# Performance work log

Measured on AMD Instinct MI355X. Metric: run time of the kernel, lower is better.

Reference implementation:

```python
import jax, jax.numpy as jnp
import numpy as np

N_VARS = 200000
M_CONS = 100000
NNZ = 1600000
HID = 128
NEG_SLOPE = 0.01  # torch F.leaky_relu default


def setup_inputs() -> dict:
    key = jax.random.key(0)
    ks = jax.random.split(key, 14)
    s = 0.05
    return {
        "primal": jax.random.normal(ks[0], (N_VARS, HID), jnp.float32),
        "last_primal": jax.random.normal(ks[1], (N_VARS, HID), jnp.float32),
        "dual": jax.random.normal(ks[2], (M_CONS, HID), jnp.float32),
        "rows": jax.random.randint(ks[3], (NNZ,), 0, M_CONS),
        "cols": jax.random.randint(ks[4], (NNZ,), 0, N_VARS),
        "vals": jax.random.normal(ks[5], (NNZ,), jnp.float32),
        "right_hand_side": jax.random.normal(ks[6], (M_CONS, HID), jnp.float32),
        "W1": jax.random.normal(ks[7], (HID, HID), jnp.float32) * s,
        "b1": jax.random.normal(ks[8], (HID,), jnp.float32) * s,
        "W2": jax.random.normal(ks[9], (HID, HID), jnp.float32) * s,
        "b2": jax.random.normal(ks[10], (HID,), jnp.float32) * s,
        "W3": jax.random.normal(ks[11], (HID, HID), jnp.float32) * s,
        "b3": jax.random.normal(ks[12], (HID,), jnp.float32) * s,
        "sigma": jnp.asarray(2.0, jnp.float32),
    }


def reference(primal, last_primal, dual, rows, cols, vals, right_hand_side,
              W1, b1, W2, b2, W3, b3, sigma):
    # X = Theta2(primal) - Theta3(last_primal): [n_vars, hid]
    X = (primal @ W2.T + b2) - (last_primal @ W3.T + b3)
    # sparse.mm(A_coo, X): gather source rows, scale by nnz vals, scatter-add to constraint rows
    msgs = vals[:, None] * X[cols]                      # [nnz, hid]
    AX = jax.ops.segment_sum(msgs, rows, num_segments=M_CONS)  # [m_cons, hid]
    pre = (dual @ W1.T + b1) + sigma * (AX - right_hand_side)
    return jnp.where(pre >= 0, pre, NEG_SLOPE * pre)
```

## Files before the change

kernel.cpp:

```cpp
#include <hip/hip_runtime.h>

#define HID 128
#define NEG_SLOPE 0.01f
#define NB 256
#define CHUNK 2048
#define MAX_RB 512
#define CAP 8192

typedef __attribute__((ext_vector_type(8))) short short8;
typedef __attribute__((ext_vector_type(4))) float f32x4;
typedef __attribute__((ext_vector_type(4))) unsigned u32x4;

__device__ inline unsigned short f2bfu(float f) {
    unsigned u = __float_as_uint(f);
    u += 0x7fff + ((u >> 16) & 1);
    return (unsigned short)(u >> 16);
}
__device__ inline float bf2f_lo(unsigned x) { return __uint_as_float((x & 0xffffu) << 16); }
__device__ inline float bf2f_hi(unsigned x) { return __uint_as_float(x & 0xffff0000u); }

__device__ inline unsigned cvtpk(float lo, float hi) {
    unsigned r;
    asm("v_cvt_pk_bf16_f32 %0, %1, %2" : "=v"(r) : "v"(lo), "v"(hi));
    return r;
}

#define MFMA_SW(accv, wfrag, xfrag) \
    asm("v_mfma_f32_16x16x32_bf16 %0, %1, %2, %0" : "+v"(accv) : "v"(wfrag), "v"(xfrag))

__global__ __launch_bounds__(256) void k_prep(
    const float* __restrict__ W1, const float* __restrict__ W2, const float* __restrict__ W3,
    unsigned short* __restrict__ Wcat, short8* __restrict__ W1F)
{
    int gid = blockIdx.x * 256 + threadIdx.x;
    if (gid < 128 * 256) {
        int n = gid >> 8, k = gid & 255;
        float v = (k < 128) ? W2[n * 128 + k] : -W3[n * 128 + (k - 128)];
        Wcat[gid] = f2bfu(v);
    } else if (gid < 128 * 256 + 2048) {
        int e = gid - 128 * 256;
        int lane = e & 63, ks = (e >> 6) & 3, nb = e >> 8;
        int row = nb * 16 + (lane & 15);
        int k0 = ks * 32 + ((lane >> 4) << 3);
        short8 v;
        #pragma unroll
        for (int j = 0; j < 8; ++j)
            v[j] = (short)f2bfu(W1[row * 128 + k0 + j]);
        W1F[e] = v;
    }
}

__device__ inline void load_a(const float* __restrict__ Ap, long rowbase, int nrows_tot,
                              int rrow, int rcol, float4 (&araw)[2][8])
{
    const float4 z4 = {0.f, 0.f, 0.f, 0.f};
    #pragma unroll
    for (int rg = 0; rg < 2; ++rg) {
        long row = rowbase + rrow + rg * 16;
        const float4* rp = (const float4*)(Ap + row * HID + rcol);
        if (row < nrows_tot) {
            #pragma unroll
            for (int ks = 0; ks < 4; ++ks) {
                araw[rg][ks * 2 + 0] = rp[ks * 8 + 0];
                araw[rg][ks * 2 + 1] = rp[ks * 8 + 1];
            }
        } else {
            #pragma unroll
            for (int u = 0; u < 8; ++u) araw[rg][u] = z4;
        }
    }
}

__device__ inline void conv_a(const float4 (&araw)[2][8], u32x4 (&af)[2][4])
{
    #pragma unroll
    for (int rg = 0; rg < 2; ++rg)
        #pragma unroll
        for (int ks = 0; ks < 4; ++ks) {
            float4 x0 = araw[rg][ks * 2 + 0], x1 = araw[rg][ks * 2 + 1];
            af[rg][ks][0] = cvtpk(x0.x, x0.y);
            af[rg][ks][1] = cvtpk(x0.z, x0.w);
            af[rg][ks][2] = cvtpk(x1.x, x1.y);
            af[rg][ks][3] = cvtpk(x1.z, x1.w);
        }
}

__device__ inline void mfma_half(f32x4 (&acc)[2][8], const u32x4 (&af)[2][4],
                                 const short8* Blds, int base, int l)
{
    #pragma unroll
    for (int ks = 0; ks < 4; ++ks)
        #pragma unroll
        for (int nb = 0; nb < 8; ++nb) {
            short8 bv = Blds[base + (nb * 4 + ks) * 64 + l];
            MFMA_SW(acc[0][nb], bv, af[0][ks]);
            MFMA_SW(acc[1][nb], bv, af[1][ks]);
        }
}

__global__ __launch_bounds__(256, 2) void k_theta_bfill(
    const float* __restrict__ primal, const float* __restrict__ lastp,
    const short8* __restrict__ Wcat,
    const float* __restrict__ b2, const float* __restrict__ b3,
    unsigned short* __restrict__ Xb, int nvars, int ntiles, int tgrid,
    const int* __restrict__ rows, const int* __restrict__ cols, const float* __restrict__ vals,
    int* __restrict__ cursor, int2* __restrict__ tmp_rc, float* __restrict__ tmp_v, int nnz, int rb,
    const float* __restrict__ dual, const short8* __restrict__ W1F,
    const float* __restrict__ b1, const float* __restrict__ rhs,
    const float* __restrict__ sigp, unsigned short* __restrict__ predualb, int mcons, int nchunks)
{
    __shared__ short8 Blds[4096];
    const int t = threadIdx.x;

    if (blockIdx.x < (unsigned)tgrid) {
        const int l = t & 63, wv = t >> 6;
        const int rrow = wv * 32 + (l & 15);
        const int rcol = (l >> 4) << 3;
        const int colb = (l >> 4) << 2;

        float4 araw[2][8];
        const long tile0 = blockIdx.x;
        load_a(primal, tile0 * 128, nvars, rrow, rcol, araw);

        #pragma unroll
        for (int i = 0; i < 16; ++i) {
            int e = t + i * 256;
            int lane = e & 63, ks = (e >> 6) & 3, nb = (e >> 8) & 7, hf = e >> 11;
            int row = nb * 16 + (lane & 15);
            int col8 = (hf * 128 + ks * 32 + ((lane >> 4) << 3)) >> 3;
            Blds[e] = Wcat[row * 32 + col8];
        }

        float4 bias[8];
        #pragma unroll
        for (int nb = 0; nb < 8; ++nb) {
            int col = nb * 16 + colb;
            float4 p = *(const float4*)&b2[col];
            float4 q = *(const float4*)&b3[col];
            bias[nb] = make_float4(p.x - q.x, p.y - q.y, p.z - q.z, p.w - q.w);
        }

        __syncthreads();

        const f32x4 z = {0.f, 0.f, 0.f, 0.f};
        f32x4 acc[2][8];
        #pragma unroll
        for (int rg = 0; rg < 2; ++rg)
            #pragma unroll
            for (int nb = 0; nb < 8; ++nb) acc[rg][nb] = z;

        u32x4 af[2][4];

        #pragma unroll 1
        for (long tile = tile0; tile < ntiles; tile += tgrid) {
            conv_a(araw, af);
            load_a(lastp, tile * 128, nvars, rrow, rcol, araw);
            mfma_half(acc, af, Blds, 0, l);

            conv_a(araw, af);
            long nt = tile + tgrid;
            if (nt < ntiles) load_a(primal, nt * 128, nvars, rrow, rcol, araw);
            mfma_half(acc, af, Blds, 2048, l);

            asm volatile("s_nop 7\ns_nop 7");
            #pragma unroll
            for (int rg = 0; rg < 2; ++rg) {
                long row = tile * 128 + rrow + rg * 16;
                if (row < nvars) {
                    #pragma unroll
                    for (int nb = 0; nb < 8; ++nb) {
                        uint2 w;
                        w.x = cvtpk(acc[rg][nb][0] + bias[nb].x, acc[rg][nb][1] + bias[nb].y);
                        w.y = cvtpk(acc[rg][nb][2] + bias[nb].z, acc[rg][nb][3] + bias[nb].w);
                        *(uint2*)&Xb[row * HID + nb * 16 + colb] = w;
                    }
                }
                #pragma unroll
                for (int nb = 0; nb < 8; ++nb) acc[rg][nb] = z;
            }
        }
    } else if (blockIdx.x < (unsigned)(tgrid + nchunks)) {
        int* hist  = (int*)Blds;
        int* basep = hist + NB;
        int cb = blockIdx.x - tgrid;
        long cbase = (long)cb * CHUNK;
        hist[t] = 0;
        __syncthreads();

        int r[8], c[8], b[8], loc[8];
        float v[8];
        #pragma unroll
        for (int i = 0; i < 8; ++i) {
            long e = cbase + i * 256 + t;
            int locv = -1; int bi = 0; int ri = 0, ci = 0; float vi = 0.f;
            if (e < nnz) {
                ri = rows[e]; ci = cols[e]; vi = vals[e];
                bi = ri / rb;
                locv = atomicAdd(&hist[bi], 1);
            }
            r[i] = ri; c[i] = ci; v[i] = vi; b[i] = bi; loc[i] = locv;
        }
        __syncthreads();
        if (hist[t] > 0) basep[t] = atomicAdd(&cursor[t], hist[t]);
        __syncthreads();
        #pragma unroll
        for (int i = 0; i < 8; ++i) {
            if (loc[i] >= 0) {
                int o = basep[b[i]] + loc[i];
                if (o < CAP) {
                    long slot = (long)b[i] * CAP + o;
                    tmp_rc[slot] = make_int2(r[i], c[i]);
                    tmp_v[slot]  = v[i];
                }
            }
        }
    } else {
        const int l = t & 63, wv = t >> 6;
        const int rrow = wv * 32 + (l & 15);
        const int rcol = (l >> 4) << 3;
        const int colb = (l >> 4) << 2;
        const float sigma = *sigp;
        const long rowbase = (long)(blockIdx.x - tgrid - nchunks) * 128;

        float4 araw[2][8];
        load_a(dual, rowbase, mcons, rrow, rcol, araw);

        u32x4 af[2][4];
        conv_a(araw, af);

        const f32x4 z = {0.f, 0.f, 0.f, 0.f};
        f32x4 acc[2][8];
        #pragma unroll
        for (int rg = 0; rg < 2; ++rg)
            #pragma unroll
            for (int nb = 0; nb < 8; ++nb) acc[rg][nb] = z;

        #pragma unroll
        for (int ks = 0; ks < 4; ++ks)
            #pragma unroll
            for (int nb = 0; nb < 8; ++nb) {
                short8 bv = W1F[(nb * 4 + ks) * 64 + l];
                MFMA_SW(acc[0][nb], bv, af[0][ks]);
                MFMA_SW(acc[1][nb], bv, af[1][ks]);
            }
        asm volatile("s_nop 7\ns_nop 7");

        float4 bias[8];
        #pragma unroll
        for (int nb = 0; nb < 8; ++nb)
            bias[nb] = *(const float4*)&b1[nb * 16 + colb];

        #pragma unroll
        for (int rg = 0; rg < 2; ++rg) {
            long row = rowbase + rrow + rg * 16;
            if (row < mcons) {
                #pragma unroll
                for (int nb = 0; nb < 8; ++nb) {
                    long idx = row * HID + nb * 16 + colb;
                    float4 r4 = *(const float4*)&rhs[idx];
                    uint2 w;
                    w.x = cvtpk(acc[rg][nb][0] + bias[nb].x - sigma * r4.x,
                                acc[rg][nb][1] + bias[nb].y - sigma * r4.y);
                    w.y = cvtpk(acc[rg][nb][2] + bias[nb].z - sigma * r4.z,
                                acc[rg][nb][3] + bias[nb].w - sigma * r4.w);
                    *(uint2*)&predualb[idx] = w;
                }
            }
        }
    }
}

__global__ __launch_bounds__(256) void k_csr(
    const int2* __restrict__ tmp_rc, const float* __restrict__ tmp_v,
    const int* __restrict__ bucket_fill,
    int* __restrict__ rowstart, int* __restrict__ count, int2* __restrict__ pairs,
    int m, int rb)
{
    __shared__ int cnt[MAX_RB];
    __shared__ int cur[MAX_RB];
    int b = blockIdx.x, t = threadIdx.x;
    int row0 = b * rb;
    int nrows = m - row0; if (nrows > rb) nrows = rb;
    if (nrows <= 0) return;

    for (int i = t; i < nrows; i += 256) cnt[i] = 0;
    __syncthreads();

    long e0 = (long)b * CAP;
    int fill = bucket_fill[b]; if (fill > CAP) fill = CAP;
    long e1 = e0 + fill;
    for (long e = e0 + t; e < e1; e += 256)
        atomicAdd(&cnt[tmp_rc[e].x - row0], 1);
    __syncthreads();

    if (t == 0) {
        int run = (int)e0;
        for (int i = 0; i < nrows; ++i) { cur[i] = run; run += cnt[i]; }
    }
    __syncthreads();

    for (int i = t; i < nrows; i += 256) {
        rowstart[row0 + i] = cur[i];
        count[row0 + i]    = cnt[i];
    }
    __syncthreads();

    for (long e = e0 + t; e < e1; e += 256) {
        int2 rc = tmp_rc[e];
        float vv = tmp_v[e];
        int slot = atomicAdd(&cur[rc.x - row0], 1);
        pairs[slot] = make_int2(rc.y, __float_as_int(vv));
    }
}

__global__ __launch_bounds__(256) void k_segsum(
    const int2* __restrict__ pairs, const int* __restrict__ rowstart, const int* __restrict__ count,
    const unsigned short* __restrict__ Xb, const unsigned short* __restrict__ predualb,
    const float* __restrict__ sigp, float* __restrict__ out, int m)
{
    int w = (blockIdx.x * 256 + threadIdx.x) >> 6;
    int lane = threadIdx.x & 63;
    int q = lane >> 4;
    int sub = lane & 15;
    int row = w * 4 + q;
    bool valid = row < m;
    int start = valid ? rowstart[row] : 0;
    int cnt   = valid ? count[row]    : 0;

    int c0 = __shfl(cnt, 0);
    int c1 = __shfl(cnt, 16);
    int c2 = __shfl(cnt, 32);
    int c3 = __shfl(cnt, 48);
    int cmax = max(max(c0, c1), max(c2, c3));

    const unsigned short* xb = Xb + sub * 8;

    float a0 = 0.f, a1 = 0.f, a2 = 0.f, a3 = 0.f;
    float a4 = 0.f, a5 = 0.f, a6 = 0.f, a7 = 0.f;
    for (int j = 0; j < cmax; j += 8) {
        int2 p[8]; u32x4 x[8];
        #pragma unroll
        for (int u = 0; u < 8; ++u) {
            bool act = (j + u) < cnt;
            int2 pv = make_int2(0, 0);
            if (act) pv = pairs[start + j + u];
            p[u] = pv;
        }
        #pragma unroll
        for (int u = 0; u < 8; ++u)
            x[u] = *(const u32x4*)(xb + (size_t)p[u].x * HID);
        #pragma unroll
        for (int u = 0; u < 8; ++u) {
            float v = __int_as_float(p[u].y);
            a0 += v * bf2f_lo(x[u][0]); a1 += v * bf2f_hi(x[u][0]);
            a2 += v * bf2f_lo(x[u][1]); a3 += v * bf2f_hi(x[u][1]);
            a4 += v * bf2f_lo(x[u][2]); a5 += v * bf2f_hi(x[u][2]);
            a6 += v * bf2f_lo(x[u][3]); a7 += v * bf2f_hi(x[u][3]);
        }
    }
    if (valid) {
        float sg = *sigp;
        long base = (size_t)row * HID + sub * 8;
        u32x4 pd = *(const u32x4*)&predualb[base];
        float4 o0, o1;
        o0.x = bf2f_lo(pd[0]) + sg * a0;
        o0.y = bf2f_hi(pd[0]) + sg * a1;
        o0.z = bf2f_lo(pd[1]) + sg * a2;
        o0.w = bf2f_hi(pd[1]) + sg * a3;
        o1.x = bf2f_lo(pd[2]) + sg * a4;
        o1.y = bf2f_hi(pd[2]) + sg * a5;
        o1.z = bf2f_lo(pd[3]) + sg * a6;
        o1.w = bf2f_hi(pd[3]) + sg * a7;
        o0.x = (o0.x >= 0.f) ? o0.x : NEG_SLOPE * o0.x;
        o0.y = (o0.y >= 0.f) ? o0.y : NEG_SLOPE * o0.y;
        o0.z = (o0.z >= 0.f) ? o0.z : NEG_SLOPE * o0.z;
        o0.w = (o0.w >= 0.f) ? o0.w : NEG_SLOPE * o0.w;
        o1.x = (o1.x >= 0.f) ? o1.x : NEG_SLOPE * o1.x;
        o1.y = (o1.y >= 0.f) ? o1.y : NEG_SLOPE * o1.y;
        o1.z = (o1.z >= 0.f) ? o1.z : NEG_SLOPE * o1.z;
        o1.w = (o1.w >= 0.f) ? o1.w : NEG_SLOPE * o1.w;
        *(float4*)&out[base]     = o0;
        *(float4*)&out[base + 4] = o1;
    }
}

extern "C" void kernel_launch(void* const* d_in, const int* in_sizes, int n_in,
                              void* d_out, int out_size, void* d_ws, size_t ws_size,
                              hipStream_t stream) {
    const float* primal = (const float*)d_in[0];
    const float* lastp  = (const float*)d_in[1];
    const float* dual   = (const float*)d_in[2];
    const int*   rows   = (const int*)d_in[3];
    const int*   cols   = (const int*)d_in[4];
    const float* vals   = (const float*)d_in[5];
    const float* rhs    = (const float*)d_in[6];
    const float* W1     = (const float*)d_in[7];
    const float* b1     = (const float*)d_in[8];
    const float* W2     = (const float*)d_in[9];
    const float* b2     = (const float*)d_in[10];
    const float* W3     = (const float*)d_in[11];
    const float* b3     = (const float*)d_in[12];
    const float* sigp   = (const float*)d_in[13];

    const int nvars = in_sizes[0] / HID;
    const int mcons = in_sizes[2] / HID;
    const int nnz   = in_sizes[3];
    const int rb    = (mcons + NB - 1) / NB;

    float* out = (float*)d_out;

    char* wsb = (char*)d_ws;
    unsigned short* Xb = (unsigned short*)wsb;
    size_t off = (size_t)nvars * HID * sizeof(unsigned short);
    int2* pairs   = (int2*)(wsb + off);  off += (size_t)NB * CAP * sizeof(int2);
    int2* tmp_rc  = (int2*)(wsb + off);  off += (size_t)NB * CAP * sizeof(int2);
    float* tmp_v  = (float*)(wsb + off); off += (size_t)NB * CAP * sizeof(float);
    unsigned short* predualb = (unsigned short*)(wsb + off);
    off += (size_t)mcons * HID * sizeof(unsigned short);
    unsigned short* Wcat = (unsigned short*)(wsb + off); off += 128 * 256 * 2;
    short8* W1F   = (short8*)(wsb + off); off += 2048 * sizeof(short8);
    int* count    = (int*)(wsb + off); off += (size_t)mcons * sizeof(int);
    int* rowstart = (int*)(wsb + off); off += (size_t)mcons * sizeof(int);
    int* cursor   = (int*)(wsb + off); off += NB * sizeof(int);

    hipMemsetAsync(cursor, 0, NB * sizeof(int), stream);

    k_prep<<<136, 256, 0, stream>>>(W1, W2, W3, Wcat, W1F);

    const int ntiles = (nvars + 127) / 128;
    const int tgrid = 512;
    const int nchunks = (nnz + CHUNK - 1) / CHUNK;
    const int pblocks = (mcons + 127) / 128;
    k_theta_bfill<<<tgrid + nchunks + pblocks, 256, 0, stream>>>(
        primal, lastp, (const short8*)Wcat, b2, b3, Xb, nvars, ntiles, tgrid,
        rows, cols, vals, cursor, tmp_rc, tmp_v, nnz, rb,
        dual, W1F, b1, rhs, sigp, predualb, mcons, nchunks);

    k_csr<<<NB, 256, 0, stream>>>(tmp_rc, tmp_v, cursor,
                                  rowstart, count, pairs, mcons, rb);

    int nwaves = (mcons + 3) / 4;
    k_segsum<<<(nwaves + 3) / 4, 256, 0, stream>>>(
        pairs, rowstart, count, Xb, predualb, sigp, out, mcons);
}
```

Measured before the change: 218.8 us.

## Fuse CSR build and segment sum into one LDS-bucketed finalize kernel

Measured after the change: 203.6 us. 6.9% less time.

```diff
diff --git a/kernel.cpp b/kernel.cpp
--- a/kernel.cpp
+++ b/kernel.cpp
@@ -2,10 +2,10 @@
 
 #define HID 128
 #define NEG_SLOPE 0.01f
-#define NB 256
+#define NBK 2048
 #define CHUNK 2048
-#define MAX_RB 512
-#define CAP 8192
+#define CAPK 1024
+#define MAX_RB 64
 
 typedef __attribute__((ext_vector_type(8))) short short8;
 typedef __attribute__((ext_vector_type(4))) float f32x4;
@@ -181,10 +181,11 @@
         }
     } else if (blockIdx.x < (unsigned)(tgrid + nchunks)) {
         int* hist  = (int*)Blds;
-        int* basep = hist + NB;
+        int* basep = hist + NBK;
         int cb = blockIdx.x - tgrid;
         long cbase = (long)cb * CHUNK;
-        hist[t] = 0;
+        #pragma unroll
+        for (int i = 0; i < NBK / 256; ++i) hist[t + i * 256] = 0;
         __syncthreads();
 
         int r[8], c[8], b[8], loc[8];
@@ -201,14 +202,18 @@
             r[i] = ri; c[i] = ci; v[i] = vi; b[i] = bi; loc[i] = locv;
         }
         __syncthreads();
-        if (hist[t] > 0) basep[t] = atomicAdd(&cursor[t], hist[t]);
+        #pragma unroll
+        for (int i = 0; i < NBK / 256; ++i) {
+            int bi = t + i * 256;
+            if (hist[bi] > 0) basep[bi] = atomicAdd(&cursor[bi], hist[bi]);
+        }
         __syncthreads();
         #pragma unroll
         for (int i = 0; i < 8; ++i) {
             if (loc[i] >= 0) {
                 int o = basep[b[i]] + loc[i];
-                if (o < CAP) {
-                    long slot = (long)b[i] * CAP + o;
+                if (o < CAPK) {
+                    long slot = (long)b[i] * CAPK + o;
                     tmp_rc[slot] = make_int2(r[i], c[i]);
                     tmp_v[slot]  = v[i];
                 }
@@ -270,117 +275,95 @@
     }
 }
 
-__global__ __launch_bounds__(256) void k_csr(
+__global__ __launch_bounds__(256) void k_segfin(
     const int2* __restrict__ tmp_rc, const float* __restrict__ tmp_v,
-    const int* __restrict__ bucket_fill,
-    int* __restrict__ rowstart, int* __restrict__ count, int2* __restrict__ pairs,
-    int m, int rb)
-{
-    __shared__ int cnt[MAX_RB];
-    __shared__ int cur[MAX_RB];
-    int b = blockIdx.x, t = threadIdx.x;
-    int row0 = b * rb;
+    const int* __restrict__ cursor,
+    const unsigned short* __restrict__ Xb, const unsigned short* __restrict__ predualb,
+    const float* __restrict__ sigp, float* __restrict__ out, int m, int rb)
+{
+    __shared__ int2 pairsL[CAPK];
+    __shared__ int cntL[MAX_RB], startL[MAX_RB], curL[MAX_RB];
+    const int b = blockIdx.x, t = threadIdx.x;
+    const int row0 = b * rb;
     int nrows = m - row0; if (nrows > rb) nrows = rb;
     if (nrows <= 0) return;
-
-    for (int i = t; i < nrows; i += 256) cnt[i] = 0;
+    int fill = cursor[b]; if (fill > CAPK) fill = CAPK;
+    const long e0 = (long)b * CAPK;
+
+    for (int i = t; i < nrows; i += 256) cntL[i] = 0;
     __syncthreads();
-
-    long e0 = (long)b * CAP;
-    int fill = bucket_fill[b]; if (fill > CAP) fill = CAP;
-    long e1 = e0 + fill;
-    for (long e = e0 + t; e < e1; e += 256)
-        atomicAdd(&cnt[tmp_rc[e].x - row0], 1);
+    for (int e = t; e < fill; e += 256)
+        atomicAdd(&cntL[tmp_rc[e0 + e].x - row0], 1);
     __syncthreads();
-
     if (t == 0) {
-        int run = (int)e0;
-        for (int i = 0; i < nrows; ++i) { cur[i] = run; run += cnt[i]; }
+        int run = 0;
+        for (int i = 0; i < nrows; ++i) { startL[i] = run; curL[i] = run; run += cntL[i]; }
     }
     __syncthreads();
-
-    for (int i = t; i < nrows; i += 256) {
-        rowstart[row0 + i] = cur[i];
-        count[row0 + i]    = cnt[i];
+    for (int e = t; e < fill; e += 256) {
+        int2 rc = tmp_rc[e0 + e];
+        float vv = tmp_v[e0 + e];
+        int slot = atomicAdd(&curL[rc.x - row0], 1);
+        pairsL[slot] = make_int2(rc.y, __float_as_int(vv));
     }
     __syncthreads();
 
-    for (long e = e0 + t; e < e1; e += 256) {
-        int2 rc = tmp_rc[e];
-        float vv = tmp_v[e];
-        int slot = atomicAdd(&cur[rc.x - row0], 1);
-        pairs[slot] = make_int2(rc.y, __float_as_int(vv));
-    }
-}
-
-__global__ __launch_bounds__(256) void k_segsum(
-    const int2* __restrict__ pairs, const int* __restrict__ rowstart, const int* __restrict__ count,
-    const unsigned short* __restrict__ Xb, const unsigned short* __restrict__ predualb,
-    const float* __restrict__ sigp, float* __restrict__ out, int m)
-{
-    int w = (blockIdx.x * 256 + threadIdx.x) >> 6;
-    int lane = threadIdx.x & 63;
-    int q = lane >> 4;
-    int sub = lane & 15;
-    int row = w * 4 + q;
-    bool valid = row < m;
-    int start = valid ? rowstart[row] : 0;
-    int cnt   = valid ? count[row]    : 0;
-
-    int c0 = __shfl(cnt, 0);
-    int c1 = __shfl(cnt, 16);
-    int c2 = __shfl(cnt, 32);
-    int c3 = __shfl(cnt, 48);
-    int cmax = max(max(c0, c1), max(c2, c3));
-
+    const float sg = *sigp;
+    const int lane = t & 63, w8 = t >> 6;
+    const int q = lane >> 4, sub = lane & 15;
     const unsigned short* xb = Xb + sub * 8;
-
-    float a0 = 0.f, a1 = 0.f, a2 = 0.f, a3 = 0.f;
-    float a4 = 0.f, a5 = 0.f, a6 = 0.f, a7 = 0.f;
-    for (int j = 0; j < cmax; j += 8) {
-        int2 p[8]; u32x4 x[8];
-        #pragma unroll
-        for (int u = 0; u < 8; ++u) {
-            bool act = (j + u) < cnt;
-            int2 pv = make_int2(0, 0);
-            if (act) pv = pairs[start + j + u];
-            p[u] = pv;
-        }
-        #pragma unroll
-        for (int u = 0; u < 8; ++u)
-            x[u] = *(const u32x4*)(xb + (size_t)p[u].x * HID);
-        #pragma unroll
-        for (int u = 0; u < 8; ++u) {
-            float v = __int_as_float(p[u].y);
-            a0 += v * bf2f_lo(x[u][0]); a1 += v * bf2f_hi(x[u][0]);
-            a2 += v * bf2f_lo(x[u][1]); a3 += v * bf2f_hi(x[u][1]);
-            a4 += v * bf2f_lo(x[u][2]); a5 += v * bf2f_hi(x[u][2]);
-            a6 += v * bf2f_lo(x[u][3]); a7 += v * bf2f_hi(x[u][3]);
-        }
-    }
-    if (valid) {
-        float sg = *sigp;
-        long base = (size_t)row * HID + sub * 8;
-        u32x4 pd = *(const u32x4*)&predualb[base];
-        float4 o0, o1;
-        o0.x = bf2f_lo(pd[0]) + sg * a0;
-        o0.y = bf2f_hi(pd[0]) + sg * a1;
-        o0.z = bf2f_lo(pd[1]) + sg * a2;
-        o0.w = bf2f_hi(pd[1]) + sg * a3;
-        o1.x = bf2f_lo(pd[2]) + sg * a4;
-        o1.y = bf2f_hi(pd[2]) + sg * a5;
-        o1.z = bf2f_lo(pd[3]) + sg * a6;
-        o1.w = bf2f_hi(pd[3]) + sg * a7;
-        o0.x = (o0.x >= 0.f) ? o0.x : NEG_SLOPE * o0.x;
-        o0.y = (o0.y >= 0.f) ? o0.y : NEG_SLOPE * o0.y;
-        o0.z = (o0.z >= 0.f) ? o0.z : NEG_SLOPE * o0.z;
-        o0.w = (o0.w >= 0.f) ? o0.w : NEG_SLOPE * o0.w;
-        o1.x = (o1.x >= 0.f) ? o1.x : NEG_SLOPE * o1.x;
-        o1.y = (o1.y >= 0.f) ? o1.y : NEG_SLOPE * o1.y;
-        o1.z = (o1.z >= 0.f) ? o1.z : NEG_SLOPE * o1.z;
-        o1.w = (o1.w >= 0.f) ? o1.w : NEG_SLOPE * o1.w;
-        *(float4*)&out[base]     = o0;
-        *(float4*)&out[base + 4] = o1;
+    const int npass = (rb + 15) / 16;
+
+    for (int pass = 0; pass < npass; ++pass) {
+        int rloc = pass * 16 + w8 * 4 + q;
+        bool valid = rloc < nrows;
+        int start = valid ? startL[rloc] : 0;
+        int cnt   = valid ? cntL[rloc]   : 0;
+
+        float a0 = 0.f, a1 = 0.f, a2 = 0.f, a3 = 0.f;
+        float a4 = 0.f, a5 = 0.f, a6 = 0.f, a7 = 0.f;
+        for (int j = 0; j < cnt; j += 8) {
+            int2 p[8]; u32x4 x[8];
+            #pragma unroll
+            for (int u = 0; u < 8; ++u) {
+                bool act = (j + u) < cnt;
+                p[u] = act ? pairsL[start + j + u] : make_int2(0, 0);
+            }
+            #pragma unroll
+            for (int u = 0; u < 8; ++u)
+                x[u] = *(const u32x4*)(xb + (size_t)p[u].x * HID);
+            #pragma unroll
+            for (int u = 0; u < 8; ++u) {
+                float v = __int_as_float(p[u].y);
+                a0 += v * bf2f_lo(x[u][0]); a1 += v * bf2f_hi(x[u][0]);
+                a2 += v * bf2f_lo(x[u][1]); a3 += v * bf2f_hi(x[u][1]);
+                a4 += v * bf2f_lo(x[u][2]); a5 += v * bf2f_hi(x[u][2]);
+                a6 += v * bf2f_lo(x[u][3]); a7 += v * bf2f_hi(x[u][3]);
+            }
+        }
+        if (valid) {
+            long base = (size_t)(row0 + rloc) * HID + sub * 8;
+            u32x4 pd = *(const u32x4*)&predualb[base];
+            float4 o0, o1;
+            o0.x = bf2f_lo(pd[0]) + sg * a0;
+            o0.y = bf2f_hi(pd[0]) + sg * a1;
+            o0.z = bf2f_lo(pd[1]) + sg * a2;
+            o0.w = bf2f_hi(pd[1]) + sg * a3;
+            o1.x = bf2f_lo(pd[2]) + sg * a4;
+            o1.y = bf2f_hi(pd[2]) + sg * a5;
+            o1.z = bf2f_lo(pd[3]) + sg * a6;
+            o1.w = bf2f_hi(pd[3]) + sg * a7;
+            o0.x = (o0.x >= 0.f) ? o0.x : NEG_SLOPE * o0.x;
+            o0.y = (o0.y >= 0.f) ? o0.y : NEG_SLOPE * o0.y;
+            o0.z = (o0.z >= 0.f) ? o0.z : NEG_SLOPE * o0.z;
+            o0.w = (o0.w >= 0.f) ? o0.w : NEG_SLOPE * o0.w;
+            o1.x = (o1.x >= 0.f) ? o1.x : NEG_SLOPE * o1.x;
+            o1.y = (o1.y >= 0.f) ? o1.y : NEG_SLOPE * o1.y;
+            o1.z = (o1.z >= 0.f) ? o1.z : NEG_SLOPE * o1.z;
+            o1.w = (o1.w >= 0.f) ? o1.w : NEG_SLOPE * o1.w;
+            *(float4*)&out[base]     = o0;
+            *(float4*)&out[base + 4] = o1;
+        }
     }
 }
 
@@ -405,25 +388,23 @@
     const int nvars = in_sizes[0] / HID;
     const int mcons = in_sizes[2] / HID;
     const int nnz   = in_sizes[3];
-    const int rb    = (mcons + NB - 1) / NB;
+    const int rb    = (mcons + NBK - 1) / NBK;
+    const int nbuckets = (mcons + rb - 1) / rb;
 
     float* out = (float*)d_out;
 
     char* wsb = (char*)d_ws;
     unsigned short* Xb = (unsigned short*)wsb;
     size_t off = (size_t)nvars * HID * sizeof(unsigned short);
-    int2* pairs   = (int2*)(wsb + off);  off += (size_t)NB * CAP * sizeof(int2);
-    int2* tmp_rc  = (int2*)(wsb + off);  off += (size_t)NB * CAP * sizeof(int2);
-    float* tmp_v  = (float*)(wsb + off); off += (size_t)NB * CAP * sizeof(float);
+    int2* tmp_rc  = (int2*)(wsb + off);  off += (size_t)NBK * CAPK * sizeof(int2);
+    float* tmp_v  = (float*)(wsb + off); off += (size_t)NBK * CAPK * sizeof(float);
     unsigned short* predualb = (unsigned short*)(wsb + off);
     off += (size_t)mcons * HID * sizeof(unsigned short);
     unsigned short* Wcat = (unsigned short*)(wsb + off); off += 128 * 256 * 2;
     short8* W1F   = (short8*)(wsb + off); off += 2048 * sizeof(short8);
-    int* count    = (int*)(wsb + off); off += (size_t)mcons * sizeof(int);
-    int* rowstart = (int*)(wsb + off); off += (size_t)mcons * sizeof(int);
-    int* cursor   = (int*)(wsb + off); off += NB * sizeof(int);
-
-    hipMemsetAsync(cursor, 0, NB * sizeof(int), stream);
+    int* cursor   = (int*)(wsb + off); off += NBK * sizeof(int);
+
+    hipMemsetAsync(cursor, 0, NBK * sizeof(int), stream);
 
     k_prep<<<136, 256, 0, stream>>>(W1, W2, W3, Wcat, W1F);
 
@@ -436,10 +417,6 @@
         rows, cols, vals, cursor, tmp_rc, tmp_v, nnz, rb,
         dual, W1F, b1, rhs, sigp, predualb, mcons, nchunks);
 
-    k_csr<<<NB, 256, 0, stream>>>(tmp_rc, tmp_v, cursor,
-                                  rowstart, count, pairs, mcons, rb);
-
-    int nwaves = (mcons + 3) / 4;
-    k_segsum<<<(nwaves + 3) / 4, 256, 0, stream>>>(
-        pairs, rowstart, count, Xb, predualb, sigp, out, mcons);
-}
+    k_segfin<<<nbuckets, 256, 0, stream>>>(
+        tmp_rc, tmp_v, cursor, Xb, predualb, sigp, out, mcons, rb);
+}
```
